# Optimization experiments

Hardware: AMD Instinct MI355X
Metric: run time of the kernel (lower is better)

## Reference

```python
import jax, jax.numpy as jnp
import numpy as np

N = 100000
E = 1600000
D_IN = 128
HID = 128
N_CLASSES = 40
NEG_SLOPE = 0.2  # PyG GATConv default
BN_EPS = 1e-5


def setup_inputs() -> dict:
    key = jax.random.key(0)
    ks = jax.random.split(key, 16)
    s = 0.1
    return {
        "x": jax.random.normal(ks[0], (N, D_IN), dtype=jnp.float32),
        "edge_index": jax.random.randint(ks[1], (2, E), 0, N, dtype=jnp.int64),
        # GAT layer 1 (in=D_IN, out=HID, heads=1)
        "W1": jax.random.normal(ks[2], (D_IN, HID), dtype=jnp.float32) * s,
        "a_src1": jax.random.normal(ks[3], (HID,), dtype=jnp.float32) * s,
        "a_dst1": jax.random.normal(ks[4], (HID,), dtype=jnp.float32) * s,
        "b1": jnp.zeros((HID,), dtype=jnp.float32),
        # GAT layer 2 (in=HID, out=HID, heads=1)
        "W2": jax.random.normal(ks[5], (HID, HID), dtype=jnp.float32) * s,
        "a_src2": jax.random.normal(ks[6], (HID,), dtype=jnp.float32) * s,
        "a_dst2": jax.random.normal(ks[7], (HID,), dtype=jnp.float32) * s,
        "b2": jnp.zeros((HID,), dtype=jnp.float32),
        # shared BatchNorm1d(HID) applied after every conv
        "gamma": jnp.ones((HID,), dtype=jnp.float32),
        "beta": jnp.zeros((HID,), dtype=jnp.float32),
        # output Linear(HID, N_CLASSES)
        "Wout": jax.random.normal(ks[8], (HID, N_CLASSES), dtype=jnp.float32) * s,
        "bout": jnp.zeros((N_CLASSES,), dtype=jnp.float32),
    }


def reference(x, edge_index, W1, a_src1, a_dst1, b1, W2, a_src2, a_dst2, b2,
              gamma, beta, Wout, bout):
    n = x.shape[0]
    loops = jnp.arange(n, dtype=edge_index.dtype)  # add_self_loops (GATConv default)
    src = jnp.concatenate([edge_index[0], loops])
    dst = jnp.concatenate([edge_index[1], loops])

    def gat_layer(h_in, W, a_s, a_d, b):
        h = h_in @ W                                   # [N, HID]
        e_src = h @ a_s                                # [N] per-node src score
        e_dst = h @ a_d                                # [N] per-node dst score
        e = jax.nn.leaky_relu(e_src[src] + e_dst[dst], NEG_SLOPE)  # [E+N]
        # segment softmax over incoming edges of each dst node
        m = jax.ops.segment_max(e, dst, num_segments=n)
        p = jnp.exp(e - m[dst])
        denom = jax.ops.segment_sum(p, dst, num_segments=n)
        alpha = p / denom[dst]
        out = jax.ops.segment_sum(alpha[:, None] * h[src], dst, num_segments=n)
        return out + b

    def bn_elu(z):
        mu = z.mean(axis=0)
        var = ((z - mu) ** 2).mean(axis=0)  # biased var (BN training mode)
        zh = (z - mu) / jnp.sqrt(var + BN_EPS) * gamma + beta
        return jax.nn.elu(zh)

    h = bn_elu(gat_layer(x, W1, a_src1, a_dst1, b1))
    h = bn_elu(gat_layer(h, W2, a_src2, a_dst2, b2))
    return h @ Wout + bout
```

## Files before the change

kernel.cpp:

```cpp
#include <hip/hip_runtime.h>

#define NNODES 100000
#define NEDGES 1600000
#define ET (NEDGES + NNODES)
#define NBUCK 196
#define NEG 0.2f
#define BNEPS 1e-5f
#define EPB 4096
#define NBLK_E ((ET + EPB - 1) / EPB)

typedef __attribute__((ext_vector_type(8))) short short8;
typedef __attribute__((ext_vector_type(4))) float floatx4;
typedef __attribute__((ext_vector_type(2))) float floatx2;

__device__ __forceinline__ unsigned short f2b(float x) {
    unsigned int u = __float_as_uint(x);
    u += 0x7fff + ((u >> 16) & 1);
    return (unsigned short)(u >> 16);
}
__device__ __forceinline__ float b2f(unsigned short u) {
    return __uint_as_float(((unsigned int)u) << 16);
}
__device__ __forceinline__ float blo2f(unsigned int v) {
    return __uint_as_float(v << 16);
}
__device__ __forceinline__ float bhi2f(unsigned int v) {
    return __uint_as_float(v & 0xffff0000u);
}
__device__ __forceinline__ floatx2 u2f2(unsigned int v) {
    floatx2 r;
    r.x = __uint_as_float(v << 16);
    r.y = __uint_as_float(v & 0xffff0000u);
    return r;
}

__device__ __forceinline__ int edge_src(const int* ei, int e, int w64) {
    if (e >= NEDGES) return e - NEDGES;
    return w64 ? ei[2 * e] : ei[e];
}
__device__ __forceinline__ int edge_dst(const int* ei, int e, int w64) {
    if (e >= NEDGES) return e - NEDGES;
    return w64 ? ei[2 * (NEDGES + e)] : ei[NEDGES + e];
}

__global__ void k_prep(const float* __restrict__ W1, const float* __restrict__ W2,
                       unsigned short* __restrict__ WT1, unsigned short* __restrict__ WT2,
                       const int* ei, int* flag, int* bcnt, int* done, float* bnstat) {
    int t = blockIdx.x * 256 + threadIdx.x;
    if (blockIdx.x == 0) {
        bcnt[threadIdx.x] = 0;
        if (threadIdx.x == 0) *done = 0;
        if (threadIdx.x == 1) {
            int is64 = 1;
            for (int j = 1; j < 16; j += 2)
                if (ei[j] != 0) is64 = 0;
            *flag = is64;
        }
    } else if (blockIdx.x == 1) {
        bnstat[threadIdx.x] = 0.f;
    } else if (blockIdx.x == 2) {
        bnstat[256 + threadIdx.x] = 0.f;
    }
    int k = t >> 7, n = t & 127;
    WT1[n * 128 + k] = f2b(W1[t]);
    WT2[n * 128 + k] = f2b(W2[t]);
}

__global__ __launch_bounds__(256) void k_bhist(const int* __restrict__ ei,
                                               const int* flag, int* bcnt,
                                               int* done, int* bbase, int* bcur) {
    __shared__ int lc[256];
    __shared__ int lastf;
    int t = threadIdx.x;
    lc[t] = 0;
    __syncthreads();
    int w64 = *flag;
    int base = blockIdx.x * EPB;
    for (int j = 0; j < EPB / 512; j++) {
        int e = base + j * 512 + t * 2;
        if (e + 1 < NEDGES) {
            int d0, d1;
            if (w64) {
                int4 dv = *(const int4*)&ei[2 * (NEDGES + e)];
                d0 = dv.x; d1 = dv.z;
            } else {
                int2 dv = *(const int2*)&ei[NEDGES + e];
                d0 = dv.x; d1 = dv.y;
            }
            atomicAdd(&lc[d0 >> 9], 1);
            atomicAdd(&lc[d1 >> 9], 1);
        } else {
            for (int k = 0; k < 2; k++) {
                int ee = e + k;
                if (ee < ET) atomicAdd(&lc[edge_dst(ei, ee, w64) >> 9], 1);
            }
        }
    }
    __syncthreads();
    if (t < NBUCK && lc[t]) atomicAdd(&bcnt[t], lc[t]);
    __threadfence();
    __syncthreads();
    if (t == 0) lastf = (atomicAdd(done, 1) == gridDim.x - 1) ? 1 : 0;
    __syncthreads();
    if (!lastf) return;
    int v = (t < NBUCK) ? atomicAdd(&bcnt[t], 0) : 0;
    __syncthreads();
    lc[t] = v;
    __syncthreads();
    for (int off = 1; off < 256; off <<= 1) {
        int add = (t >= off) ? lc[t - off] : 0;
        __syncthreads();
        lc[t] += add;
        __syncthreads();
    }
    int excl = lc[t] - v;
    if (t < NBUCK) { bbase[t] = excl; bcur[t] = excl; }
    if (t == NBUCK - 1) bbase[NBUCK] = excl + v;
}

__global__ __launch_bounds__(256) void k_bscatter(const int* __restrict__ ei,
                                                  const int* flag, int* bcur,
                                                  int* __restrict__ pairs) {
    __shared__ int lc[256];
    __shared__ int lbase[256];
    int t = threadIdx.x;
    lc[t] = 0;
    __syncthreads();
    int w64 = *flag;
    int base = blockIdx.x * EPB;
    for (int j = 0; j < EPB / 512; j++) {
        int e = base + j * 512 + t * 2;
        if (e + 1 < NEDGES) {
            int d0, d1;
            if (w64) {
                int4 dv = *(const int4*)&ei[2 * (NEDGES + e)];
                d0 = dv.x; d1 = dv.z;
            } else {
                int2 dv = *(const int2*)&ei[NEDGES + e];
                d0 = dv.x; d1 = dv.y;
            }
            atomicAdd(&lc[d0 >> 9], 1);
            atomicAdd(&lc[d1 >> 9], 1);
        } else {
            for (int k = 0; k < 2; k++) {
                int ee = e + k;
                if (ee < ET) atomicAdd(&lc[edge_dst(ei, ee, w64) >> 9], 1);
            }
        }
    }
    __syncthreads();
    if (t < NBUCK && lc[t]) lbase[t] = atomicAdd(&bcur[t], lc[t]);
    __syncthreads();
    for (int j = 0; j < EPB / 512; j++) {
        int e = base + j * 512 + t * 2;
        if (e + 1 < NEDGES) {
            int s0, s1, d0, d1;
            if (w64) {
                int4 sv = *(const int4*)&ei[2 * e];
                int4 dv = *(const int4*)&ei[2 * (NEDGES + e)];
                s0 = sv.x; s1 = sv.z; d0 = dv.x; d1 = dv.z;
            } else {
                int2 sv = *(const int2*)&ei[e];
                int2 dv = *(const int2*)&ei[NEDGES + e];
                s0 = sv.x; s1 = sv.y; d0 = dv.x; d1 = dv.y;
            }
            int p0 = atomicAdd(&lbase[d0 >> 9], 1);
            pairs[p0] = (s0 << 9) | (d0 & 511);
            int p1 = atomicAdd(&lbase[d1 >> 9], 1);
            pairs[p1] = (s1 << 9) | (d1 & 511);
        } else {
            for (int k = 0; k < 2; k++) {
                int ee = e + k;
                if (ee < ET) {
                    int src = edge_src(ei, ee, w64);
                    int dst = edge_dst(ei, ee, w64);
                    int pos = atomicAdd(&lbase[dst >> 9], 1);
                    pairs[pos] = (src << 9) | (dst & 511);
                }
            }
        }
    }
}

__global__ __launch_bounds__(256) void k_bsort(const int* __restrict__ pairs,
                                               const int* __restrict__ bbase,
                                               int* __restrict__ rowptr,
                                               int* __restrict__ srcs) {
    __shared__ int ncnt[512];
    __shared__ int nbase[512];
    __shared__ int stmp[256];
    int b = blockIdx.x, t = threadIdx.x;
    ncnt[t] = 0; ncnt[t + 256] = 0;
    __syncthreads();
    int s0 = bbase[b], s1 = bbase[b + 1];
    for (int i = s0 + t; i < s1; i += 256)
        atomicAdd(&ncnt[pairs[i] & 511], 1);
    __syncthreads();
    int c0 = ncnt[2 * t], c1 = ncnt[2 * t + 1];
    int s = c0 + c1;
    stmp[t] = s;
    __syncthreads();
    for (int off = 1; off < 256; off <<= 1) {
        int add = (t >= off) ? stmp[t - off] : 0;
        __syncthreads();
        stmp[t] += add;
        __syncthreads();
    }
    int excl = stmp[t] - s;
    nbase[2 * t] = excl;
    nbase[2 * t + 1] = excl + c0;
    __syncthreads();
    for (int l = t; l < 512; l += 256) {
        int node = b * 512 + l;
        if (node <= NNODES) rowptr[node] = s0 + nbase[l];
        ncnt[l] = nbase[l];
    }
    __syncthreads();
    for (int i = s0 + t; i < s1; i += 256) {
        int pr = pairs[i];
        int off = atomicAdd(&ncnt[pr & 511], 1);
        srcs[s0 + off] = ((unsigned int)pr) >> 9;
    }
}

template<bool BN>
__global__ __launch_bounds__(256) void k_gemm(const void* __restrict__ Ain,
        const unsigned short* __restrict__ WTg,
        const float* __restrict__ sums, const float* __restrict__ sqs,
        const float* __restrict__ gamma, const float* __restrict__ beta,
        const float* __restrict__ a_s, const float* __restrict__ a_d,
        float* __restrict__ es, float* __restrict__ ed,
        unsigned short* __restrict__ hB, int n) {
    __shared__ unsigned short lA[64][136];
    __shared__ unsigned short lW[128][136];
    __shared__ float las[128], lad[128];
    __shared__ float lsc[128], lsh[128];
    int t = threadIdx.x;
    int row0 = blockIdx.x * 64;
    if (t < 128) { las[t] = a_s[t]; lad[t] = a_d[t]; }
    if (BN && t < 128) {
        float mu = sums[t] * (1.f / NNODES);
        float var = fmaxf(sqs[t] * (1.f / NNODES) - mu * mu, 0.f);
        float s = gamma[t] * rsqrtf(var + BNEPS);
        lsc[t] = s;
        lsh[t] = beta[t] - mu * s;
    }

    const uint4* wt4 = (const uint4*)WTg;
#pragma unroll
    for (int j = 0; j < 8; j++) {
        int idx = t + j * 256;
        *(uint4*)&lW[idx >> 4][(idx & 15) * 8] = wt4[idx];
    }
    if (BN) __syncthreads();

    if (BN) {
        const uint4* Ab = (const uint4*)Ain;
#pragma unroll
        for (int j = 0; j < 4; j++) {
            int idx = t + j * 256;
            int r = idx >> 4, seg = idx & 15;
            uint4 v = make_uint4(0, 0, 0, 0);
            if (row0 + r < n) v = Ab[(size_t)(row0 + r) * 16 + seg];
            float f[8];
            f[0] = blo2f(v.x); f[1] = bhi2f(v.x);
            f[2] = blo2f(v.y); f[3] = bhi2f(v.y);
            f[4] = blo2f(v.z); f[5] = bhi2f(v.z);
            f[6] = blo2f(v.w); f[7] = bhi2f(v.w);
            ushort4 u0, u1;
            unsigned short us[8];
#pragma unroll
            for (int k = 0; k < 8; k++) {
                int c = seg * 8 + k;
                float z = fmaf(f[k], lsc[c], lsh[c]);
                z = z > 0.f ? z : __expf(z) - 1.f;
                us[k] = f2b(z);
            }
            u0.x = us[0]; u0.y = us[1]; u0.z = us[2]; u0.w = us[3];
            u1.x = us[4]; u1.y = us[5]; u1.z = us[6]; u1.w = us[7];
            *(ushort4*)&lA[r][seg * 8] = u0;
            *(ushort4*)&lA[r][seg * 8 + 4] = u1;
        }
    } else {
        const float* Af = (const float*)Ain;
#pragma unroll
        for (int j = 0; j < 8; j++) {
            int idx = t + j * 256;
            int r = idx >> 5, c4 = idx & 31;
            float4 v = make_float4(0.f, 0.f, 0.f, 0.f);
            if (row0 + r < n) v = ((const float4*)Af)[(size_t)(row0 + r) * 32 + c4];
            ushort4 u;
            u.x = f2b(v.x); u.y = f2b(v.y); u.z = f2b(v.z); u.w = f2b(v.w);
            *(ushort4*)&lA[r][c4 * 4] = u;
        }
    }
    __syncthreads();

    int w = t >> 6, lane = t & 63;
    int m = lane & 15, q = lane >> 4;
    int arow = w * 16 + m;
    floatx4 acc[8];
#pragma unroll
    for (int ct = 0; ct < 8; ct++) acc[ct] = (floatx4)0.0f;

#pragma unroll
    for (int kt = 0; kt < 4; kt++) {
        int kb = kt * 32 + q * 8;
        short8 af = *(const short8*)&lA[arow][kb];
#pragma unroll
        for (int ct = 0; ct < 8; ct++) {
            short8 bf = *(const short8*)&lW[ct * 16 + m][kb];
            acc[ct] = __builtin_amdgcn_mfma_f32_16x16x32_bf16(af, bf, acc[ct], 0, 0, 0);
        }
    }

    __syncthreads();
#pragma unroll
    for (int ct = 0; ct < 8; ct++)
#pragma unroll
        for (int r = 0; r < 4; r++)
            lA[w * 16 + q * 4 + r][ct * 16 + m] = f2b(acc[ct][r]);
#pragma unroll
    for (int j = 0; j < 4; j++) {
        int idx = lane + j * 64;
        int r = idx >> 4, seg = idx & 15;
        int grow = row0 + w * 16 + r;
        if (grow < n) {
            uint4 v = *(const uint4*)&lA[w * 16 + r][seg * 8];
            ((uint4*)hB)[(size_t)grow * 16 + seg] = v;
        }
    }
    __syncthreads();
    int r = t >> 2, q4 = t & 3;
    float s1 = 0.f, s2 = 0.f;
#pragma unroll
    for (int k = 0; k < 32; k++) {
        int c = q4 * 32 + k;
        float v = b2f(lA[r][c]);
        s1 += v * las[c];
        s2 += v * lad[c];
    }
    s1 += __shfl_xor(s1, 1, 64); s1 += __shfl_xor(s1, 2, 64);
    s2 += __shfl_xor(s2, 1, 64); s2 += __shfl_xor(s2, 2, 64);
    if (q4 == 0 && row0 + r < n) { es[row0 + r] = s1; ed[row0 + r] = s2; }
}

__global__ __launch_bounds__(256) void k_attn(const unsigned short* __restrict__ hB,
                                              const int* __restrict__ srcs,
                                              const int* __restrict__ rowptr,
                                              const float* __restrict__ es,
                                              const float* __restrict__ ed,
                                              const float* __restrict__ bias,
                                              unsigned short* __restrict__ haggB, int n) {
    int w = (blockIdx.x * 256 + threadIdx.x) >> 5;
    if (w >= n) return;
    int lane32 = threadIdx.x & 31;
    int g = lane32 >> 4, l16 = lane32 & 15;
    int base = threadIdx.x & 32;
    int start = rowptr[w], end = rowptr[w + 1];
    float edv = ed[w];
    const uint4* hp4 = (const uint4*)hB;
    floatx2 a0 = {0.f, 0.f}, a1 = {0.f, 0.f}, a2 = {0.f, 0.f}, a3 = {0.f, 0.f};
    float den = 0.f;

    for (int chunk = start; chunk < end; chunk += 32) {
        int i = chunk + lane32;
        int sv = 0; float pv = 0.f;
        if (i < end) {
            sv = srcs[i];
            float e = es[sv] + edv;
            e = e > 0.f ? e : NEG * e;
            pv = __expf(e);
            den += pv;
        }
        int cnt = min(32, end - chunk);
        for (int j = 0; j < cnt; j += 4) {
            int   s0 = __shfl(sv, base + j + g, 64);
            float p0 = __shfl(pv, base + j + g, 64);
            int   s1 = __shfl(sv, base + j + 2 + g, 64);
            float p1 = __shfl(pv, base + j + 2 + g, 64);
            if (p0 != 0.f) {
                uint4 h0 = hp4[(size_t)s0 * 16 + l16];
                floatx2 P = {p0, p0};
                a0 += P * u2f2(h0.x); a1 += P * u2f2(h0.y);
                a2 += P * u2f2(h0.z); a3 += P * u2f2(h0.w);
            }
            if (p1 != 0.f) {
                uint4 h1 = hp4[(size_t)s1 * 16 + l16];
                floatx2 P = {p1, p1};
                a0 += P * u2f2(h1.x); a1 += P * u2f2(h1.y);
                a2 += P * u2f2(h1.z); a3 += P * u2f2(h1.w);
            }
        }
    }
    den += __shfl_xor(den, 1, 64);  den += __shfl_xor(den, 2, 64);
    den += __shfl_xor(den, 4, 64);  den += __shfl_xor(den, 8, 64);
    den += __shfl_xor(den, 16, 64);
    a0.x += __shfl_xor(a0.x, 16, 64); a0.y += __shfl_xor(a0.y, 16, 64);
    a1.x += __shfl_xor(a1.x, 16, 64); a1.y += __shfl_xor(a1.y, 16, 64);
    a2.x += __shfl_xor(a2.x, 16, 64); a2.y += __shfl_xor(a2.y, 16, 64);
    a3.x += __shfl_xor(a3.x, 16, 64); a3.y += __shfl_xor(a3.y, 16, 64);
    if (g == 0) {
        float inv = 1.f / den;
        const float2* b2p = (const float2*)bias;
        float2 c0 = b2p[l16 * 4 + 0], c1 = b2p[l16 * 4 + 1];
        float2 c2 = b2p[l16 * 4 + 2], c3 = b2p[l16 * 4 + 3];
        uint4 o;
        o.x = (unsigned int)f2b(fmaf(a0.x, inv, c0.x)) |
              ((unsigned int)f2b(fmaf(a0.y, inv, c0.y)) << 16);
        o.y = (unsigned int)f2b(fmaf(a1.x, inv, c1.x)) |
              ((unsigned int)f2b(fmaf(a1.y, inv, c1.y)) << 16);
        o.z = (unsigned int)f2b(fmaf(a2.x, inv, c2.x)) |
              ((unsigned int)f2b(fmaf(a2.y, inv, c2.y)) << 16);
        o.w = (unsigned int)f2b(fmaf(a3.x, inv, c3.x)) |
              ((unsigned int)f2b(fmaf(a3.y, inv, c3.y)) << 16);
        ((uint4*)haggB)[(size_t)w * 16 + l16] = o;
    }
}

__global__ __launch_bounds__(256) void k_bnstats(const unsigned short* __restrict__ hin,
                                                 float* sums, float* sqs, int n) {
    __shared__ float red[4][256];
    int t = threadIdx.x;
    int c2 = t & 63, quarter = t >> 6;
    int r0 = blockIdx.x * 512;
    int rend = min(r0 + 512, n);
    const unsigned int* hp = (const unsigned int*)hin;
    float s0 = 0.f, q0 = 0.f, s1 = 0.f, q1 = 0.f;
    for (int r = r0 + quarter; r < rend; r += 4) {
        unsigned int v = hp[(size_t)r * 64 + c2];
        float a = blo2f(v), b = bhi2f(v);
        s0 += a; q0 += a * a;
        s1 += b; q1 += b * b;
    }
    *(float4*)&red[quarter][c2 * 4] = make_float4(s0, q0, s1, q1);
    __syncthreads();
    float v = red[0][t] + red[1][t] + red[2][t] + red[3][t];
    int c2i = t >> 2, k = t & 3;
    int ch = c2i * 2 + (k >> 1);
    if (k & 1) atomicAdd(&sqs[ch], v);
    else       atomicAdd(&sums[ch], v);
}

__global__ __launch_bounds__(256) void k_outgemm(const unsigned short* __restrict__ h,
                                                 const float* __restrict__ sums,
                                                 const float* __restrict__ sqs,
                                                 const float* __restrict__ gamma,
                                                 const float* __restrict__ beta,
                                                 const float* __restrict__ Wout,
                                                 const float* __restrict__ bout,
                                                 float* __restrict__ out, int n) {
    __shared__ float lwT[40][128];
    __shared__ float lh[64][132];
    __shared__ float lb[40];
    __shared__ float lsc[128], lsh[128];
    int t = threadIdx.x;
    if (t < 128) {
        float mu = sums[t] * (1.f / NNODES);
        float var = fmaxf(sqs[t] * (1.f / NNODES) - mu * mu, 0.f);
        float s = gamma[t] * rsqrtf(var + BNEPS);
        lsc[t] = s;
        lsh[t] = beta[t] - mu * s;
    }
    for (int idx = t; idx < 128 * 40; idx += 256) {
        int r = idx / 40, c = idx % 40;
        lwT[c][r] = Wout[idx];
    }
    if (t < 40) lb[t] = bout[t];
    __syncthreads();
    int n0 = blockIdx.x * 64;
    const uint4* hb4 = (const uint4*)h;
#pragma unroll
    for (int j = 0; j < 4; j++) {
        int idx = t + j * 256;
        int r = idx >> 4, seg = idx & 15;
        uint4 v = make_uint4(0, 0, 0, 0);
        if (n0 + r < n) v = hb4[(size_t)(n0 + r) * 16 + seg];
        float f[8];
        f[0] = blo2f(v.x); f[1] = bhi2f(v.x);
        f[2] = blo2f(v.y); f[3] = bhi2f(v.y);
        f[4] = blo2f(v.z); f[5] = bhi2f(v.z);
        f[6] = blo2f(v.w); f[7] = bhi2f(v.w);
#pragma unroll
        for (int k = 0; k < 8; k++) {
            int c = seg * 8 + k;
            float z = fmaf(f[k], lsc[c], lsh[c]);
            z = z > 0.f ? z : __expf(z) - 1.f;
            lh[r][c] = z;
        }
    }
    __syncthreads();
    int nl = t & 63, g = t >> 6;
    int row = n0 + nl;
    if (row >= n) return;
    float acc[10] = {};
    for (int k = 0; k < 128; k += 4) {
        float4 hv = *(const float4*)&lh[nl][k];
#pragma unroll
        for (int j = 0; j < 10; j++) {
            float4 wv = *(const float4*)&lwT[g * 10 + j][k];
            acc[j] += hv.x * wv.x + hv.y * wv.y + hv.z * wv.z + hv.w * wv.w;
        }
    }
#pragma unroll
    for (int j = 0; j < 10; j++)
        out[(size_t)row * 40 + g * 10 + j] = acc[j] + lb[g * 10 + j];
}

extern "C" void kernel_launch(void* const* d_in, const int* in_sizes, int n_in,
                              void* d_out, int out_size, void* d_ws, size_t ws_size,
                              hipStream_t stream) {
    const float* x      = (const float*)d_in[0];
    const int*   ei     = (const int*)d_in[1];
    const float* W1     = (const float*)d_in[2];
    const float* a_src1 = (const float*)d_in[3];
    const float* a_dst1 = (const float*)d_in[4];
    const float* b1     = (const float*)d_in[5];
    const float* W2     = (const float*)d_in[6];
    const float* a_src2 = (const float*)d_in[7];
    const float* a_dst2 = (const float*)d_in[8];
    const float* b2     = (const float*)d_in[9];
    const float* gamma  = (const float*)d_in[10];
    const float* beta   = (const float*)d_in[11];
    const float* Wout   = (const float*)d_in[12];
    const float* bout   = (const float*)d_in[13];
    float* out = (float*)d_out;

    char* p = (char*)d_ws;
    auto alloc = [&](size_t bytes) -> void* {
        void* r = (void*)p;
        p += (bytes + 255) & ~(size_t)255;
        return r;
    };
    unsigned short* hB    = (unsigned short*)alloc((size_t)NNODES * 128 * 2);
    unsigned short* haggB = (unsigned short*)alloc((size_t)NNODES * 128 * 2);
    float* es     = (float*)alloc((size_t)NNODES * 4);
    float* ed     = (float*)alloc((size_t)NNODES * 4);
    int*   pairs  = (int*)alloc((size_t)ET * 4);
    int*   srcs   = (int*)alloc((size_t)ET * 4);
    int*   rowptr = (int*)alloc((size_t)(NNODES + 1) * 4);
    int*   bcnt   = (int*)alloc(256 * 4);
    int*   bbase  = (int*)alloc(256 * 4);
    int*   bcur   = (int*)alloc(256 * 4);
    float* bnstat = (float*)alloc(4 * 128 * 4);
    unsigned short* WT1 = (unsigned short*)alloc(128 * 128 * 2);
    unsigned short* WT2 = (unsigned short*)alloc(128 * 128 * 2);
    int*   flag   = (int*)alloc(4);
    int*   done   = (int*)alloc(4);

    float* sum1 = bnstat, *sq1 = bnstat + 128, *sum2 = bnstat + 256, *sq2 = bnstat + 384;

    k_prep<<<64, 256, 0, stream>>>(W1, W2, WT1, WT2, ei, flag, bcnt, done, bnstat);
    k_bhist<<<NBLK_E, 256, 0, stream>>>(ei, flag, bcnt, done, bbase, bcur);
    k_bscatter<<<NBLK_E, 256, 0, stream>>>(ei, flag, bcur, pairs);
    k_bsort<<<NBUCK, 256, 0, stream>>>(pairs, bbase, rowptr, srcs);

    const int GB = (NNODES + 63) / 64;
    const int AB = NNODES / 8;
    const int SB = (NNODES + 511) / 512;

    k_gemm<false><<<GB, 256, 0, stream>>>(x, WT1, nullptr, nullptr, nullptr, nullptr,
                                          a_src1, a_dst1, es, ed, hB, NNODES);
    k_attn<<<AB, 256, 0, stream>>>(hB, srcs, rowptr, es, ed, b1, haggB, NNODES);
    k_bnstats<<<SB, 256, 0, stream>>>(haggB, sum1, sq1, NNODES);

    k_gemm<true><<<GB, 256, 0, stream>>>(haggB, WT2, sum1, sq1, gamma, beta,
                                         a_src2, a_dst2, es, ed, hB, NNODES);
    k_attn<<<AB, 256, 0, stream>>>(hB, srcs, rowptr, es, ed, b2, haggB, NNODES);
    k_bnstats<<<SB, 256, 0, stream>>>(haggB, sum2, sq2, NNODES);

    k_outgemm<<<GB, 256, 0, stream>>>(haggB, sum2, sq2, gamma, beta, Wout, bout, out, NNODES);

    (void)in_sizes; (void)n_in; (void)out_size; (void)ws_size;
}
```

Before: 477.7 us.

## Use finer 128-node sort buckets, 128-row GEMM tiles, and smaller BN stat blocks

The destination bucketing in the CSR build is refined from 512-node to 128-node buckets (782 buckets), so k_bsort launches more blocks with smaller per-block scans. The node GEMM now processes 128 rows per block, with each wave computing two 16-row MFMA tiles that share the same weight fragments. The attention score dot products use paired bf16 loads. BN stats blocks now cover 256 rows instead of 512. These changes aim to raise parallelism in the sort and improve weight reuse in the GEMM, at the cost of more global bucket atomics, a larger LDS footprint and fewer GEMM blocks.

```diff
diff --git a/kernel.cpp b/kernel.cpp
--- a/kernel.cpp
+++ b/kernel.cpp
@@ -3,7 +3,7 @@
 #define NNODES 100000
 #define NEDGES 1600000
 #define ET (NEDGES + NNODES)
-#define NBUCK 196
+#define NBUCK 782
 #define NEG 0.2f
 #define BNEPS 1e-5f
 #define EPB 4096
@@ -47,19 +47,18 @@
                        unsigned short* __restrict__ WT1, unsigned short* __restrict__ WT2,
                        const int* ei, int* flag, int* bcnt, int* done, float* bnstat) {
     int t = blockIdx.x * 256 + threadIdx.x;
-    if (blockIdx.x == 0) {
-        bcnt[threadIdx.x] = 0;
-        if (threadIdx.x == 0) *done = 0;
-        if (threadIdx.x == 1) {
-            int is64 = 1;
-            for (int j = 1; j < 16; j += 2)
-                if (ei[j] != 0) is64 = 0;
-            *flag = is64;
-        }
-    } else if (blockIdx.x == 1) {
+    if (t < 800) bcnt[t] = 0;
+    if (blockIdx.x == 4) {
         bnstat[threadIdx.x] = 0.f;
-    } else if (blockIdx.x == 2) {
+    } else if (blockIdx.x == 5) {
         bnstat[256 + threadIdx.x] = 0.f;
+    }
+    if (t == 0) *done = 0;
+    if (t == 1) {
+        int is64 = 1;
+        for (int j = 1; j < 16; j += 2)
+            if (ei[j] != 0) is64 = 0;
+        *flag = is64;
     }
     int k = t >> 7, n = t & 127;
     WT1[n * 128 + k] = f2b(W1[t]);
@@ -69,10 +68,11 @@
 __global__ __launch_bounds__(256) void k_bhist(const int* __restrict__ ei,
                                                const int* flag, int* bcnt,
                                                int* done, int* bbase, int* bcur) {
-    __shared__ int lc[256];
+    __shared__ int lc[784];
+    __shared__ int sh[256];
     __shared__ int lastf;
     int t = threadIdx.x;
-    lc[t] = 0;
+    for (int i = t; i < NBUCK; i += 256) lc[i] = 0;
     __syncthreads();
     int w64 = *flag;
     int base = blockIdx.x * EPB;
@@ -87,44 +87,55 @@
                 int2 dv = *(const int2*)&ei[NEDGES + e];
                 d0 = dv.x; d1 = dv.y;
             }
-            atomicAdd(&lc[d0 >> 9], 1);
-            atomicAdd(&lc[d1 >> 9], 1);
+            atomicAdd(&lc[d0 >> 7], 1);
+            atomicAdd(&lc[d1 >> 7], 1);
         } else {
             for (int k = 0; k < 2; k++) {
                 int ee = e + k;
-                if (ee < ET) atomicAdd(&lc[edge_dst(ei, ee, w64) >> 9], 1);
-            }
-        }
-    }
-    __syncthreads();
-    if (t < NBUCK && lc[t]) atomicAdd(&bcnt[t], lc[t]);
+                if (ee < ET) atomicAdd(&lc[edge_dst(ei, ee, w64) >> 7], 1);
+            }
+        }
+    }
+    __syncthreads();
+    for (int i = t; i < NBUCK; i += 256)
+        if (lc[i]) atomicAdd(&bcnt[i], lc[i]);
     __threadfence();
     __syncthreads();
     if (t == 0) lastf = (atomicAdd(done, 1) == gridDim.x - 1) ? 1 : 0;
     __syncthreads();
     if (!lastf) return;
-    int v = (t < NBUCK) ? atomicAdd(&bcnt[t], 0) : 0;
-    __syncthreads();
-    lc[t] = v;
+    int vals[4], pre[4], sum = 0;
+#pragma unroll
+    for (int i = 0; i < 4; i++) {
+        int id = t * 4 + i;
+        int v = (id < NBUCK) ? atomicAdd(&bcnt[id], 0) : 0;
+        pre[i] = sum; vals[i] = v; sum += v;
+    }
+    sh[t] = sum;
     __syncthreads();
     for (int off = 1; off < 256; off <<= 1) {
-        int add = (t >= off) ? lc[t - off] : 0;
+        int add = (t >= off) ? sh[t - off] : 0;
         __syncthreads();
-        lc[t] += add;
+        sh[t] += add;
         __syncthreads();
     }
-    int excl = lc[t] - v;
-    if (t < NBUCK) { bbase[t] = excl; bcur[t] = excl; }
-    if (t == NBUCK - 1) bbase[NBUCK] = excl + v;
+    int excl = sh[t] - sum;
+#pragma unroll
+    for (int i = 0; i < 4; i++) {
+        int id = t * 4 + i;
+        if (id < NBUCK) { bbase[id] = excl + pre[i]; bcur[id] = excl + pre[i]; }
+    }
+    if (t == 255) bbase[NBUCK] = sh[255];
+    (void)vals;
 }
 
 __global__ __launch_bounds__(256) void k_bscatter(const int* __restrict__ ei,
                                                   const int* flag, int* bcur,
                                                   int* __restrict__ pairs) {
-    __shared__ int lc[256];
-    __shared__ int lbase[256];
+    __shared__ int lc[784];
+    __shared__ int lbase[784];
     int t = threadIdx.x;
-    lc[t] = 0;
+    for (int i = t; i < NBUCK; i += 256) lc[i] = 0;
     __syncthreads();
     int w64 = *flag;
     int base = blockIdx.x * EPB;
@@ -139,17 +150,18 @@
                 int2 dv = *(const int2*)&ei[NEDGES + e];
                 d0 = dv.x; d1 = dv.y;
             }
-            atomicAdd(&lc[d0 >> 9], 1);
-            atomicAdd(&lc[d1 >> 9], 1);
+            atomicAdd(&lc[d0 >> 7], 1);
+            atomicAdd(&lc[d1 >> 7], 1);
         } else {
             for (int k = 0; k < 2; k++) {
                 int ee = e + k;
-                if (ee < ET) atomicAdd(&lc[edge_dst(ei, ee, w64) >> 9], 1);
-            }
-        }
-    }
-    __syncthreads();
-    if (t < NBUCK && lc[t]) lbase[t] = atomicAdd(&bcur[t], lc[t]);
+                if (ee < ET) atomicAdd(&lc[edge_dst(ei, ee, w64) >> 7], 1);
+            }
+        }
+    }
+    __syncthreads();
+    for (int i = t; i < NBUCK; i += 256)
+        if (lc[i]) lbase[i] = atomicAdd(&bcur[i], lc[i]);
     __syncthreads();
     for (int j = 0; j < EPB / 512; j++) {
         int e = base + j * 512 + t * 2;
@@ -164,18 +176,18 @@
                 int2 dv = *(const int2*)&ei[NEDGES + e];
                 s0 = sv.x; s1 = sv.y; d0 = dv.x; d1 = dv.y;
             }
-            int p0 = atomicAdd(&lbase[d0 >> 9], 1);
-            pairs[p0] = (s0 << 9) | (d0 & 511);
-            int p1 = atomicAdd(&lbase[d1 >> 9], 1);
-            pairs[p1] = (s1 << 9) | (d1 & 511);
+            int p0 = atomicAdd(&lbase[d0 >> 7], 1);
+            pairs[p0] = (s0 << 7) | (d0 & 127);
+            int p1 = atomicAdd(&lbase[d1 >> 7], 1);
+            pairs[p1] = (s1 << 7) | (d1 & 127);
         } else {
             for (int k = 0; k < 2; k++) {
                 int ee = e + k;
                 if (ee < ET) {
                     int src = edge_src(ei, ee, w64);
                     int dst = edge_dst(ei, ee, w64);
-                    int pos = atomicAdd(&lbase[dst >> 9], 1);
-                    pairs[pos] = (src << 9) | (dst & 511);
+                    int pos = atomicAdd(&lbase[dst >> 7], 1);
+                    pairs[pos] = (src << 7) | (dst & 127);
                 }
             }
         }
@@ -186,40 +198,38 @@
                                                const int* __restrict__ bbase,
                                                int* __restrict__ rowptr,
                                                int* __restrict__ srcs) {
-    __shared__ int ncnt[512];
-    __shared__ int nbase[512];
-    __shared__ int stmp[256];
+    __shared__ int ncnt[128];
+    __shared__ int nbase[128];
+    __shared__ int sscan[128];
     int b = blockIdx.x, t = threadIdx.x;
-    ncnt[t] = 0; ncnt[t + 256] = 0;
+    if (t < 128) ncnt[t] = 0;
     __syncthreads();
     int s0 = bbase[b], s1 = bbase[b + 1];
     for (int i = s0 + t; i < s1; i += 256)
-        atomicAdd(&ncnt[pairs[i] & 511], 1);
-    __syncthreads();
-    int c0 = ncnt[2 * t], c1 = ncnt[2 * t + 1];
-    int s = c0 + c1;
-    stmp[t] = s;
-    __syncthreads();
-    for (int off = 1; off < 256; off <<= 1) {
-        int add = (t >= off) ? stmp[t - off] : 0;
+        atomicAdd(&ncnt[pairs[i] & 127], 1);
+    __syncthreads();
+    int v = (t < 128) ? ncnt[t] : 0;
+    if (t < 128) sscan[t] = v;
+    __syncthreads();
+    for (int off = 1; off < 128; off <<= 1) {
+        int add = (t < 128 && t >= off) ? sscan[t - off] : 0;
         __syncthreads();
-        stmp[t] += add;
+        if (t < 128) sscan[t] += add;
         __syncthreads();
     }
-    int excl = stmp[t] - s;
-    nbase[2 * t] = excl;
-    nbase[2 * t + 1] = excl + c0;
-    __syncthreads();
-    for (int l = t; l < 512; l += 256) {
-        int node = b * 512 + l;
-        if (node <= NNODES) rowptr[node] = s0 + nbase[l];
-        ncnt[l] = nbase[l];
-    }
+    if (t < 128) {
+        int excl = sscan[t] - v;
+        nbase[t] = excl;
+        int node = b * 128 + t;
+        if (node <= NNODES) rowptr[node] = s0 + excl;
+    }
+    __syncthreads();
+    if (t < 128) ncnt[t] = nbase[t];
     __syncthreads();
     for (int i = s0 + t; i < s1; i += 256) {
         int pr = pairs[i];
-        int off = atomicAdd(&ncnt[pr & 511], 1);
-        srcs[s0 + off] = ((unsigned int)pr) >> 9;
+        int off = atomicAdd(&ncnt[pr & 127], 1);
+        srcs[s0 + off] = ((unsigned int)pr) >> 7;
     }
 }
 
@@ -231,12 +241,12 @@
         const float* __restrict__ a_s, const float* __restrict__ a_d,
         float* __restrict__ es, float* __restrict__ ed,
         unsigned short* __restrict__ hB, int n) {
-    __shared__ unsigned short lA[64][136];
+    __shared__ unsigned short lA[128][136];
     __shared__ unsigned short lW[128][136];
     __shared__ float las[128], lad[128];
     __shared__ float lsc[128], lsh[128];
     int t = threadIdx.x;
-    int row0 = blockIdx.x * 64;
+    int row0 = blockIdx.x * 128;
     if (t < 128) { las[t] = a_s[t]; lad[t] = a_d[t]; }
     if (BN && t < 128) {
         float mu = sums[t] * (1.f / NNODES);
@@ -257,7 +267,7 @@
     if (BN) {
         const uint4* Ab = (const uint4*)Ain;
 #pragma unroll
-        for (int j = 0; j < 4; j++) {
+        for (int j = 0; j < 8; j++) {
             int idx = t + j * 256;
             int r = idx >> 4, seg = idx & 15;
             uint4 v = make_uint4(0, 0, 0, 0);
@@ -267,7 +277,6 @@
             f[2] = blo2f(v.y); f[3] = bhi2f(v.y);
             f[4] = blo2f(v.z); f[5] = bhi2f(v.z);
             f[6] = blo2f(v.w); f[7] = bhi2f(v.w);
-            ushort4 u0, u1;
             unsigned short us[8];
 #pragma unroll
             for (int k = 0; k < 8; k++) {
@@ -276,6 +285,7 @@
                 z = z > 0.f ? z : __expf(z) - 1.f;
                 us[k] = f2b(z);
             }
+            ushort4 u0, u1;
             u0.x = us[0]; u0.y = us[1]; u0.z = us[2]; u0.w = us[3];
             u1.x = us[4]; u1.y = us[5]; u1.z = us[6]; u1.w = us[7];
             *(ushort4*)&lA[r][seg * 8] = u0;
@@ -284,7 +294,7 @@
     } else {
         const float* Af = (const float*)Ain;
 #pragma unroll
-        for (int j = 0; j < 8; j++) {
+        for (int j = 0; j < 16; j++) {
             int idx = t + j * 256;
             int r = idx >> 5, c4 = idx & 31;
             float4 v = make_float4(0.f, 0.f, 0.f, 0.f);
@@ -298,19 +308,21 @@
 
     int w = t >> 6, lane = t & 63;
     int m = lane & 15, q = lane >> 4;
-    int arow = w * 16 + m;
-    floatx4 acc[8];
-#pragma unroll
-    for (int ct = 0; ct < 8; ct++) acc[ct] = (floatx4)0.0f;
+    int ar0 = w * 32 + m, ar1 = w * 32 + 16 + m;
+    floatx4 acc0[8], acc1[8];
+#pragma unroll
+    for (int ct = 0; ct < 8; ct++) { acc0[ct] = (floatx4)0.0f; acc1[ct] = (floatx4)0.0f; }
 
 #pragma unroll
     for (int kt = 0; kt < 4; kt++) {
         int kb = kt * 32 + q * 8;
-        short8 af = *(const short8*)&lA[arow][kb];
+        short8 af0 = *(const short8*)&lA[ar0][kb];
+        short8 af1 = *(const short8*)&lA[ar1][kb];
 #pragma unroll
         for (int ct = 0; ct < 8; ct++) {
             short8 bf = *(const short8*)&lW[ct * 16 + m][kb];
-            acc[ct] = __builtin_amdgcn_mfma_f32_16x16x32_bf16(af, bf, acc[ct], 0, 0, 0);
+            acc0[ct] = __builtin_amdgcn_mfma_f32_16x16x32_bf16(af0, bf, acc0[ct], 0, 0, 0);
+            acc1[ct] = __builtin_amdgcn_mfma_f32_16x16x32_bf16(af1, bf, acc1[ct], 0, 0, 0);
         }
     }
 
@@ -318,31 +330,34 @@
 #pragma unroll
     for (int ct = 0; ct < 8; ct++)
 #pragma unroll
-        for (int r = 0; r < 4; r++)
-            lA[w * 16 + q * 4 + r][ct * 16 + m] = f2b(acc[ct][r]);
-#pragma unroll
-    for (int j = 0; j < 4; j++) {
-        int idx = lane + j * 64;
+        for (int r = 0; r < 4; r++) {
+            lA[w * 32 + q * 4 + r][ct * 16 + m] = f2b(acc0[ct][r]);
+            lA[w * 32 + 16 + q * 4 + r][ct * 16 + m] = f2b(acc1[ct][r]);
+        }
+    __syncthreads();
+#pragma unroll
+    for (int j = 0; j < 8; j++) {
+        int idx = t + j * 256;
         int r = idx >> 4, seg = idx & 15;
-        int grow = row0 + w * 16 + r;
+        int grow = row0 + r;
         if (grow < n) {
-            uint4 v = *(const uint4*)&lA[w * 16 + r][seg * 8];
+            uint4 v = *(const uint4*)&lA[r][seg * 8];
             ((uint4*)hB)[(size_t)grow * 16 + seg] = v;
         }
     }
-    __syncthreads();
-    int r = t >> 2, q4 = t & 3;
+    int r = t >> 1, q2 = t & 1;
     float s1 = 0.f, s2 = 0.f;
 #pragma unroll
     for (int k = 0; k < 32; k++) {
-        int c = q4 * 32 + k;
-        float v = b2f(lA[r][c]);
-        s1 += v * las[c];
-        s2 += v * lad[c];
-    }
-    s1 += __shfl_xor(s1, 1, 64); s1 += __shfl_xor(s1, 2, 64);
-    s2 += __shfl_xor(s2, 1, 64); s2 += __shfl_xor(s2, 2, 64);
-    if (q4 == 0 && row0 + r < n) { es[row0 + r] = s1; ed[row0 + r] = s2; }
+        int c = q2 * 64 + 2 * k;
+        unsigned int u = *(const unsigned int*)&lA[r][c];
+        float va = blo2f(u), vb = bhi2f(u);
+        s1 += va * las[c] + vb * las[c + 1];
+        s2 += va * lad[c] + vb * lad[c + 1];
+    }
+    s1 += __shfl_xor(s1, 1, 64);
+    s2 += __shfl_xor(s2, 1, 64);
+    if (q2 == 0 && row0 + r < n) { es[row0 + r] = s1; ed[row0 + r] = s2; }
 }
 
 __global__ __launch_bounds__(256) void k_attn(const unsigned short* __restrict__ hB,
@@ -423,8 +438,8 @@
     __shared__ float red[4][256];
     int t = threadIdx.x;
     int c2 = t & 63, quarter = t >> 6;
-    int r0 = blockIdx.x * 512;
-    int rend = min(r0 + 512, n);
+    int r0 = blockIdx.x * 256;
+    int rend = min(r0 + 256, n);
     const unsigned int* hp = (const unsigned int*)hin;
     float s0 = 0.f, q0 = 0.f, s1 = 0.f, q1 = 0.f;
     for (int r = r0 + quarter; r < rend; r += 4) {
@@ -539,9 +554,9 @@
     int*   pairs  = (int*)alloc((size_t)ET * 4);
     int*   srcs   = (int*)alloc((size_t)ET * 4);
     int*   rowptr = (int*)alloc((size_t)(NNODES + 1) * 4);
-    int*   bcnt   = (int*)alloc(256 * 4);
-    int*   bbase  = (int*)alloc(256 * 4);
-    int*   bcur   = (int*)alloc(256 * 4);
+    int*   bcnt   = (int*)alloc(800 * 4);
+    int*   bbase  = (int*)alloc(800 * 4);
+    int*   bcur   = (int*)alloc(800 * 4);
     float* bnstat = (float*)alloc(4 * 128 * 4);
     unsigned short* WT1 = (unsigned short*)alloc(128 * 128 * 2);
     unsigned short* WT2 = (unsigned short*)alloc(128 * 128 * 2);
@@ -555,9 +570,10 @@
     k_bscatter<<<NBLK_E, 256, 0, stream>>>(ei, flag, bcur, pairs);
     k_bsort<<<NBUCK, 256, 0, stream>>>(pairs, bbase, rowptr, srcs);
 
-    const int GB = (NNODES + 63) / 64;
+    const int GB = (NNODES + 127) / 128;
     const int AB = NNODES / 8;
-    const int SB = (NNODES + 511) / 512;
+    const int SB = (NNODES + 255) / 256;
+    const int OB = (NNODES + 63) / 64;
 
     k_gemm<false><<<GB, 256, 0, stream>>>(x, WT1, nullptr, nullptr, nullptr, nullptr,
                                           a_src1, a_dst1, es, ed, hB, NNODES);
@@ -569,7 +585,7 @@
     k_attn<<<AB, 256, 0, stream>>>(hB, srcs, rowptr, es, ed, b2, haggB, NNODES);
     k_bnstats<<<SB, 256, 0, stream>>>(haggB, sum2, sq2, NNODES);
 
-    k_outgemm<<<GB, 256, 0, stream>>>(haggB, sum2, sq2, gamma, beta, Wout, bout, out, NNODES);
+    k_outgemm<<<OB, 256, 0, stream>>>(haggB, sum2, sq2, gamma, beta, Wout, bout, out, NNODES);
 
     (void)in_sizes; (void)n_in; (void)out_size; (void)ws_size;
 }
```

Result: faster. 458.8 us (-4.0%).
